# Kernel tuning notes

Hardware: AMD Instinct MI355X
Metric: run time of the kernel (lower is better)

## Reference

```python
import jax, jax.numpy as jnp
import numpy as np

LOG2 = float(np.log(2.0))

def ssp(x):
    # shifted softplus used throughout SchNet
    return jax.nn.softplus(x) - LOG2

def setup_inputs() -> dict:
    key = jax.random.key(0)
    ks = jax.random.split(key, 12)
    B, Na, Nn, G, F = 16, 512, 64, 25, 128
    s = 0.05
    return {
        "x": jax.random.normal(ks[0], (B, Na, F), jnp.float32),
        "r_ij": jax.random.uniform(ks[1], (B, Na, Nn), jnp.float32),
        "f_ij": jax.random.uniform(ks[2], (B, Na, Nn, G), jnp.float32),
        "neighbours": jax.random.randint(ks[3], (B, Na, Nn), 0, Na),
        "pairwise_mask": jax.random.uniform(ks[4], (B, Na, Nn), jnp.float32),
        "W_in2f": jax.random.normal(ks[5], (F, F), jnp.float32) * s,
        "W_f1": jax.random.normal(ks[6], (G, F), jnp.float32) * s,
        "b_f1": jnp.zeros((F,), jnp.float32),
        "W_f2": jax.random.normal(ks[7], (F, F), jnp.float32) * s,
        "b_f2": jnp.zeros((F,), jnp.float32),
        "W_out": jax.random.normal(ks[8], (F, F), jnp.float32) * s,
        "b_out": jnp.zeros((F,), jnp.float32),
    }

def reference(x, r_ij, f_ij, neighbours, pairwise_mask,
              W_in2f, W_f1, b_f1, W_f2, b_f2, W_out, b_out):
    # filter_network: Dense(G->F, ssp) -> Dense(F->F)
    W = jnp.einsum('bang,gf->banf', f_ij, W_f1) + b_f1  # [B,Na,Nn,F]
    W = ssp(W)
    W = jnp.einsum('banf,fg->bang', W, W_f2) + b_f2
    # in2f (no bias)
    y = jnp.einsum('bai,if->baf', x, W_in2f)  # [B,Na,F]
    B, Na, Nn = neighbours.shape
    # gather neighbor features: y[b, neighbours[b,a,n], :]
    nbh = neighbours.reshape(B, Na * Nn, 1)
    g = jnp.take_along_axis(y, nbh, axis=1).reshape(B, Na, Nn, -1)
    # filter multiply, mask, aggregate over neighbor axis (sum, no mean)
    agg = jnp.sum(g * W * pairwise_mask[..., None], axis=2)  # [B,Na,F]
    # f2out with shifted softplus activation
    out = ssp(jnp.einsum('baf,fo->bao', agg, W_out) + b_out)
    return out
```

## Files before the change

kernel.cpp:

```cpp
#include <hip/hip_runtime.h>

typedef __attribute__((ext_vector_type(8))) short bf16x8;
typedef __attribute__((ext_vector_type(4))) float f32x4;
typedef __attribute__((ext_vector_type(4))) unsigned int u32x4;

#define LOG2F 0.69314718055994531f
#define LOG2EF 1.4426950408889634f

#define NB 16
#define NA 512
#define NN 64
#define NG 25
#define NF 128

__device__ __forceinline__ unsigned short f2bf(float x) {
    __bf16 h = (__bf16)x;
    return __builtin_bit_cast(unsigned short, h);
}
__device__ __forceinline__ float ssp2(float s) {
    float t = __builtin_amdgcn_exp2f(s);
    return fmaf(__builtin_amdgcn_logf(1.0f + t), LOG2F, -LOG2F);
}

__device__ __forceinline__ void stage_fij(const float* fp, float* sfij, int w, int lane) {
    const char* fb = (const char*)fp;
    __builtin_amdgcn_global_load_lds(
        (const __attribute__((address_space(1))) void*)(fb + w * 1024 + lane * 16),
        (__attribute__((address_space(3))) void*)((char*)sfij + w * 1024), 16, 0, 0);
    if (w < 2) {
        __builtin_amdgcn_global_load_lds(
            (const __attribute__((address_space(1))) void*)(fb + (w + 4) * 1024 + lane * 16),
            (__attribute__((address_space(3))) void*)((char*)sfij + (w + 4) * 1024), 16, 0, 0);
    }
    if (w == 3) {
        __builtin_amdgcn_global_load_lds(
            (const __attribute__((address_space(1))) void*)(fb + 6144 + lane * 4),
            (__attribute__((address_space(3))) void*)((char*)sfij + 6144), 4, 0, 0);
    }
}

#define FRAG_WF1 0
#define FRAG_WF2 4096
#define FRAG_WIN 20480
#define FRAG_WOUT 36864
#define B1S_OFF   106496
#define YBF_OFF   107008
#define AGG_OFF   2204160

__global__ __launch_bounds__(256) void k_prep(
    const float* __restrict__ Wf1, const float* __restrict__ Wf2,
    const float* __restrict__ Win, const float* __restrict__ Wout,
    const float* __restrict__ b1, char* __restrict__ ws)
{
    unsigned short* frag = (unsigned short*)ws;
    int idx = blockIdx.x * 256 + threadIdx.x;
    if (idx < 4096) {
        int j = idx & 7, lane = (idx >> 3) & 63, tc = idx >> 9;
        int f1 = tc * 16 + (lane & 15);
        int g  = (lane >> 4) * 8 + j;
        frag[idx] = (g < NG) ? f2bf(Wf1[g * NF + f1] * LOG2EF) : (unsigned short)0;
    } else if (idx < 20480) {
        int t = idx - 4096;
        int j = t & 7, lane = (t >> 3) & 63, ks = (t >> 9) & 3, tn = t >> 11;
        int f = tn * 16 + (lane & 15);
        int k = ks * 32 + (lane >> 4) * 8 + j;
        frag[idx] = f2bf(Wf2[k * NF + f]);
    } else if (idx < 36864) {
        int t = idx - 20480;
        int j = t & 7, lane = (t >> 3) & 63, ks = (t >> 9) & 3, tn = t >> 11;
        int f = tn * 16 + (lane & 15);
        int k = ks * 32 + (lane >> 4) * 8 + j;
        frag[idx] = f2bf(Win[k * NF + f]);
    } else if (idx < 53248) {
        int t = idx - 36864;
        int j = t & 7, lane = (t >> 3) & 63, ks = (t >> 9) & 3, tn = t >> 11;
        int f = tn * 16 + (lane & 15);
        int k = ks * 32 + (lane >> 4) * 8 + j;
        frag[idx] = f2bf(Wout[k * NF + f]);
    } else if (idx < 53376) {
        ((float*)(ws + B1S_OFF))[idx - 53248] = b1[idx - 53248] * LOG2EF;
    }
}

__global__ __launch_bounds__(256) void k_in2f(
    const float* __restrict__ x, const unsigned short* __restrict__ frag,
    unsigned short* __restrict__ ybf)
{
    const unsigned short* winfrag = frag + FRAG_WIN;
    const int lane = threadIdx.x & 63, w = threadIdx.x >> 6;
    const int rowbase = blockIdx.x * 32;
    f32x4 acc[2][2];
    f32x4 z = {0.f, 0.f, 0.f, 0.f};
    acc[0][0] = z; acc[0][1] = z; acc[1][0] = z; acc[1][1] = z;
#pragma unroll
    for (int ks = 0; ks < 4; ++ks) {
        bf16x8 a[2];
#pragma unroll
        for (int tm = 0; tm < 2; ++tm) {
            int row = rowbase + tm * 16 + (lane & 15);
            int k0  = ks * 32 + (lane >> 4) * 8;
            const float* p = x + (size_t)row * NF + k0;
            float4 v0 = *(const float4*)p;
            float4 v1 = *(const float4*)(p + 4);
            bf16x8 t;
            t[0] = (short)f2bf(v0.x); t[1] = (short)f2bf(v0.y);
            t[2] = (short)f2bf(v0.z); t[3] = (short)f2bf(v0.w);
            t[4] = (short)f2bf(v1.x); t[5] = (short)f2bf(v1.y);
            t[6] = (short)f2bf(v1.z); t[7] = (short)f2bf(v1.w);
            a[tm] = t;
        }
#pragma unroll
        for (int tn = 0; tn < 2; ++tn) {
            bf16x8 bfr = *(const bf16x8*)(winfrag + ((((w * 2 + tn) * 4 + ks) * 64) + lane) * 8);
#pragma unroll
            for (int tm = 0; tm < 2; ++tm)
                acc[tm][tn] = __builtin_amdgcn_mfma_f32_16x16x32_bf16(a[tm], bfr, acc[tm][tn], 0, 0, 0);
        }
    }
#pragma unroll
    for (int tm = 0; tm < 2; ++tm)
#pragma unroll
        for (int tn = 0; tn < 2; ++tn)
#pragma unroll
            for (int r = 0; r < 4; ++r) {
                int row = rowbase + tm * 16 + (lane >> 4) * 4 + r;
                int f   = w * 32 + tn * 16 + (lane & 15);
                ybf[(size_t)row * NF + f] = f2bf(acc[tm][tn][r]);
            }
}

__global__ __launch_bounds__(256, 4) void k_cfconv(
    const float* __restrict__ fij, const int* __restrict__ nbh,
    const float* __restrict__ mask, const float* __restrict__ b1s,
    const float* __restrict__ b2, const unsigned short* __restrict__ frag,
    const unsigned short* __restrict__ ybf, float* __restrict__ agg)
{
    __shared__ alignas(16) float sfij[1600];
    __shared__ alignas(16) unsigned short sW1T[8192];
    __shared__ alignas(16) float smask[128];
    __shared__ alignas(16) int   snbh[128];

    const int tid = threadIdx.x, lane = tid & 63, w = tid >> 6;
    const int g = lane >> 4, lc = lane & 15;
    const int a0 = blockIdx.x * 2;
    const int bidx = a0 >> 9;
    const int fbase = w * 32;
    const int fc0 = fbase + lc;

    if (tid < 128) {
        smask[tid] = mask[(size_t)a0 * NN + tid];
        snbh[tid]  = nbh[(size_t)a0 * NN + tid];
    }

    stage_fij(fij + (size_t)a0 * (NN * NG), sfij, w, lane);

    const unsigned short* wf1frag = frag + FRAG_WF1;
    const unsigned short* wf2frag = frag + FRAG_WF2;
    bf16x8 afr[2], vb[4];
    f32x4  rg[8];
#pragma unroll
    for (int i = 0; i < 2; ++i)
        afr[i] = *(const bf16x8*)(wf1frag + (((2 * w + i) * 64) + lane) * 8);
    f32x4 ci[2];
#pragma unroll
    for (int i = 0; i < 2; ++i)
        ci[i] = *(const f32x4*)(b1s + (2 * w + i) * 16 + g * 4);
    const float bias0 = b2[fc0], bias1 = b2[fc0 + 16];
    const unsigned short* yb = ybf + (size_t)bidx * NA * NF;

    __syncthreads();

#pragma unroll
    for (int a = 0; a < 2; ++a) {
        {
            const int g0 = g * 8;
            const unsigned int m0 = (g == 3) ? 0x0000FFFFu : 0xFFFFFFFFu;
            const unsigned int m1 = (g == 3) ? 0u : 0xFFFFFFFFu;
#pragma unroll
            for (int tn = 0; tn < 4; ++tn) {
                int n = tn * 16 + lc;
                const float* p = sfij + n * NG + g0;
                bf16x8 t;
                t[0] = (short)f2bf(p[0]); t[1] = (short)f2bf(p[1]);
                t[2] = (short)f2bf(p[2]); t[3] = (short)f2bf(p[3]);
                t[4] = (short)f2bf(p[4]); t[5] = (short)f2bf(p[5]);
                t[6] = (short)f2bf(p[6]); t[7] = (short)f2bf(p[7]);
                u32x4 tv = __builtin_bit_cast(u32x4, t);
                tv[0] &= m0; tv[1] &= m1; tv[2] &= m1; tv[3] &= m1;
                vb[tn] = __builtin_bit_cast(bf16x8, tv);
            }
        }

        if (a == 0) {
            __syncthreads();
            stage_fij(fij + (size_t)(a0 + 1) * (NN * NG), sfij, w, lane);
        }

#pragma unroll
        for (int i = 0; i < 2; ++i)
#pragma unroll
            for (int tn = 0; tn < 4; ++tn)
                rg[i * 4 + tn] = __builtin_amdgcn_mfma_f32_16x16x32_bf16(afr[i], vb[tn], ci[i], 0, 0, 0);

#pragma unroll
        for (int i = 0; i < 2; ++i) {
            int c0 = (2 * w + i) * 16 + g * 4;
#pragma unroll
            for (int tn = 0; tn < 4; ++tn) {
                int n = tn * 16 + lc;
                ushort4 pk;
#pragma unroll
                for (int r = 0; r < 4; ++r)
                    ((unsigned short*)&pk)[r] = f2bf(ssp2(rg[i * 4 + tn][r]));
                *(ushort4*)((char*)sW1T + n * 256 + ((c0 * 2) ^ ((n & 7) << 4))) = pk;
            }
        }
        __syncthreads();

#pragma unroll
        for (int tm = 0; tm < 4; ++tm) {
            rg[tm * 2 + 0] = f32x4{bias0, bias0, bias0, bias0};
            rg[tm * 2 + 1] = f32x4{bias1, bias1, bias1, bias1};
        }
#pragma unroll
        for (int ks = 0; ks < 4; ++ks) {
#pragma unroll
            for (int tm = 0; tm < 4; ++tm) {
                int n  = tm * 16 + lc;
                int kb = ks * 64 + g * 16;
                vb[tm] = *(const bf16x8*)((char*)sW1T + n * 256 + (kb ^ ((n & 7) << 4)));
            }
#pragma unroll
            for (int tnl = 0; tnl < 2; ++tnl) {
                int tn = w * 2 + tnl;
                bf16x8 bf2 = *(const bf16x8*)(wf2frag + (((tn * 4 + ks) * 64) + lane) * 8);
#pragma unroll
                for (int tm = 0; tm < 4; ++tm)
                    rg[tm * 2 + tnl] = __builtin_amdgcn_mfma_f32_16x16x32_bf16(vb[tm], bf2, rg[tm * 2 + tnl], 0, 0, 0);
            }
        }

        {
            const float* sm = smask + a * 64;
            const int*   sn = snbh + a * 64;
            float aggv0 = 0.f, aggv1 = 0.f;
#pragma unroll
            for (int tm = 0; tm < 4; ++tm) {
                f32x4 m4 = *(const f32x4*)(sm + tm * 16 + g * 4);
                int4  nb4 = *(const int4*)(sn + tm * 16 + g * 4);
#pragma unroll
                for (int r = 0; r < 4; ++r) {
                    int yrow = (r == 0) ? nb4.x : (r == 1) ? nb4.y : (r == 2) ? nb4.z : nb4.w;
                    const unsigned short* yp = yb + (size_t)yrow * NF + fc0;
                    float y0 = __builtin_bit_cast(float, (unsigned int)yp[0] << 16);
                    float y1 = __builtin_bit_cast(float, (unsigned int)yp[16] << 16);
                    aggv0 = fmaf(rg[tm * 2 + 0][r] * m4[r], y0, aggv0);
                    aggv1 = fmaf(rg[tm * 2 + 1][r] * m4[r], y1, aggv1);
                }
            }
            aggv0 += __shfl_xor(aggv0, 16); aggv1 += __shfl_xor(aggv1, 16);
            aggv0 += __shfl_xor(aggv0, 32); aggv1 += __shfl_xor(aggv1, 32);
            if (lane < 16) {
                float* ap = agg + (size_t)(a0 + a) * NF + fbase;
                ap[lane] = aggv0;
                ap[16 + lane] = aggv1;
            }
        }

        if (a == 0) __syncthreads();
    }
}

__global__ __launch_bounds__(256) void k_out(
    const float* __restrict__ agg, const unsigned short* __restrict__ frag,
    const float* __restrict__ bout, float* __restrict__ out)
{
    const unsigned short* wofrag = frag + FRAG_WOUT;
    const int lane = threadIdx.x & 63, w = threadIdx.x >> 6;
    const int rowbase = blockIdx.x * 32;
    const int f0 = w * 32 + (lane & 15);
    const float bo0 = bout[f0], bo1 = bout[f0 + 16];
    f32x4 acc[2][2];
    acc[0][0] = f32x4{bo0, bo0, bo0, bo0};
    acc[1][0] = f32x4{bo0, bo0, bo0, bo0};
    acc[0][1] = f32x4{bo1, bo1, bo1, bo1};
    acc[1][1] = f32x4{bo1, bo1, bo1, bo1};
#pragma unroll
    for (int ks = 0; ks < 4; ++ks) {
        bf16x8 a[2];
#pragma unroll
        for (int tm = 0; tm < 2; ++tm) {
            int row = rowbase + tm * 16 + (lane & 15);
            int k0  = ks * 32 + (lane >> 4) * 8;
            const float* p = agg + (size_t)row * NF + k0;
            float4 v0 = *(const float4*)p;
            float4 v1 = *(const float4*)(p + 4);
            bf16x8 t;
            t[0] = (short)f2bf(v0.x); t[1] = (short)f2bf(v0.y);
            t[2] = (short)f2bf(v0.z); t[3] = (short)f2bf(v0.w);
            t[4] = (short)f2bf(v1.x); t[5] = (short)f2bf(v1.y);
            t[6] = (short)f2bf(v1.z); t[7] = (short)f2bf(v1.w);
            a[tm] = t;
        }
#pragma unroll
        for (int tn = 0; tn < 2; ++tn) {
            bf16x8 bfr = *(const bf16x8*)(wofrag + ((((w * 2 + tn) * 4 + ks) * 64) + lane) * 8);
#pragma unroll
            for (int tm = 0; tm < 2; ++tm)
                acc[tm][tn] = __builtin_amdgcn_mfma_f32_16x16x32_bf16(a[tm], bfr, acc[tm][tn], 0, 0, 0);
        }
    }
    float lg2 = LOG2EF;
#pragma unroll
    for (int tm = 0; tm < 2; ++tm)
#pragma unroll
        for (int tn = 0; tn < 2; ++tn)
#pragma unroll
            for (int r = 0; r < 4; ++r) {
                int row = rowbase + tm * 16 + (lane >> 4) * 4 + r;
                int f   = w * 32 + tn * 16 + (lane & 15);
                out[(size_t)row * NF + f] = ssp2(acc[tm][tn][r] * lg2);
            }
}

extern "C" void kernel_launch(void* const* d_in, const int* in_sizes, int n_in,
                              void* d_out, int out_size, void* d_ws, size_t ws_size,
                              hipStream_t stream)
{
    (void)in_sizes; (void)n_in; (void)out_size; (void)ws_size;
    const float* x    = (const float*)d_in[0];
    const float* fij  = (const float*)d_in[2];
    const int*   nbh  = (const int*)d_in[3];
    const float* mask = (const float*)d_in[4];
    const float* Win  = (const float*)d_in[5];
    const float* Wf1  = (const float*)d_in[6];
    const float* b1   = (const float*)d_in[7];
    const float* Wf2  = (const float*)d_in[8];
    const float* b2   = (const float*)d_in[9];
    const float* Wout = (const float*)d_in[10];
    const float* bout = (const float*)d_in[11];
    float* out = (float*)d_out;

    char* ws = (char*)d_ws;
    unsigned short* frag = (unsigned short*)ws;
    const float*    b1s  = (const float*)(ws + B1S_OFF);
    unsigned short* ybf  = (unsigned short*)(ws + YBF_OFF);
    float*          agg  = (float*)(ws + AGG_OFF);

    k_prep  <<<209,  256, 0, stream>>>(Wf1, Wf2, Win, Wout, b1, ws);
    k_in2f  <<<256,  256, 0, stream>>>(x, frag, ybf);
    k_cfconv<<<4096, 256, 0, stream>>>(fij, nbh, mask, b1s, b2, frag, ybf, agg);
    k_out   <<<256,  256, 0, stream>>>(agg, frag, bout, out);
}
```

Baseline: 59.49 us.

## Process both atoms concurrently with two waves per atom in cfconv kernel

```diff
diff --git a/kernel.cpp b/kernel.cpp
--- a/kernel.cpp
+++ b/kernel.cpp
@@ -13,29 +13,35 @@
 #define NG 25
 #define NF 128
 
+#define AS1 __attribute__((address_space(1)))
+#define AS3 __attribute__((address_space(3)))
+
 __device__ __forceinline__ unsigned short f2bf(float x) {
     __bf16 h = (__bf16)x;
     return __builtin_bit_cast(unsigned short, h);
 }
+__device__ __forceinline__ float bf2f(unsigned short h) {
+    union { unsigned int u; float f; } c; c.u = ((unsigned int)h) << 16;
+    return c.f;
+}
 __device__ __forceinline__ float ssp2(float s) {
     float t = __builtin_amdgcn_exp2f(s);
     return fmaf(__builtin_amdgcn_logf(1.0f + t), LOG2F, -LOG2F);
 }
 
-__device__ __forceinline__ void stage_fij(const float* fp, float* sfij, int w, int lane) {
+__device__ __forceinline__ void stage_fij2(const float* fp, char* dst, int wp, int lane) {
     const char* fb = (const char*)fp;
-    __builtin_amdgcn_global_load_lds(
-        (const __attribute__((address_space(1))) void*)(fb + w * 1024 + lane * 16),
-        (__attribute__((address_space(3))) void*)((char*)sfij + w * 1024), 16, 0, 0);
-    if (w < 2) {
+#pragma unroll
+    for (int c = 0; c < 3; ++c) {
+        int chunk = wp * 3 + c;
         __builtin_amdgcn_global_load_lds(
-            (const __attribute__((address_space(1))) void*)(fb + (w + 4) * 1024 + lane * 16),
-            (__attribute__((address_space(3))) void*)((char*)sfij + (w + 4) * 1024), 16, 0, 0);
-    }
-    if (w == 3) {
+            (const AS1 void*)(fb + chunk * 1024 + lane * 16),
+            (AS3 void*)(dst + chunk * 1024), 16, 0, 0);
+    }
+    if (wp == 1) {
         __builtin_amdgcn_global_load_lds(
-            (const __attribute__((address_space(1))) void*)(fb + 6144 + lane * 4),
-            (__attribute__((address_space(3))) void*)((char*)sfij + 6144), 4, 0, 0);
+            (const AS1 void*)(fb + 6144 + lane * 4),
+            (AS3 void*)(dst + 6144), 4, 0, 0);
     }
 }
 
@@ -135,139 +141,147 @@
     const float* __restrict__ b2, const unsigned short* __restrict__ frag,
     const unsigned short* __restrict__ ybf, float* __restrict__ agg)
 {
-    __shared__ alignas(16) float sfij[1600];
-    __shared__ alignas(16) unsigned short sW1T[8192];
-    __shared__ alignas(16) float smask[128];
-    __shared__ alignas(16) int   snbh[128];
+    __shared__ alignas(16) char smem[33792];
+    float* smask = (float*)(smem + 32768);
+    int*   snbh  = (int*)(smem + 33280);
 
     const int tid = threadIdx.x, lane = tid & 63, w = tid >> 6;
+    const int wp = w & 1, at = w >> 1;
     const int g = lane >> 4, lc = lane & 15;
     const int a0 = blockIdx.x * 2;
+    const int atom = a0 + at;
     const int bidx = a0 >> 9;
-    const int fbase = w * 32;
-    const int fc0 = fbase + lc;
 
     if (tid < 128) {
         smask[tid] = mask[(size_t)a0 * NN + tid];
         snbh[tid]  = nbh[(size_t)a0 * NN + tid];
     }
 
-    stage_fij(fij + (size_t)a0 * (NN * NG), sfij, w, lane);
+    char* myW1T = smem + at * 16384;
+    stage_fij2(fij + (size_t)atom * (NN * NG), myW1T, wp, lane);
 
     const unsigned short* wf1frag = frag + FRAG_WF1;
     const unsigned short* wf2frag = frag + FRAG_WF2;
-    bf16x8 afr[2], vb[4];
-    f32x4  rg[8];
-#pragma unroll
-    for (int i = 0; i < 2; ++i)
-        afr[i] = *(const bf16x8*)(wf1frag + (((2 * w + i) * 64) + lane) * 8);
-    f32x4 ci[2];
-#pragma unroll
-    for (int i = 0; i < 2; ++i)
-        ci[i] = *(const f32x4*)(b1s + (2 * w + i) * 16 + g * 4);
-    const float bias0 = b2[fc0], bias1 = b2[fc0 + 16];
-    const unsigned short* yb = ybf + (size_t)bidx * NA * NF;
+    bf16x8 afr[4];
+#pragma unroll
+    for (int i = 0; i < 4; ++i)
+        afr[i] = *(const bf16x8*)(wf1frag + (((wp * 4 + i) * 64) + lane) * 8);
+    float bb[4];
+#pragma unroll
+    for (int tf = 0; tf < 4; ++tf)
+        bb[tf] = b2[wp * 64 + tf * 16 + lc];
 
     __syncthreads();
 
-#pragma unroll
-    for (int a = 0; a < 2; ++a) {
-        {
-            const int g0 = g * 8;
-            const unsigned int m0 = (g == 3) ? 0x0000FFFFu : 0xFFFFFFFFu;
-            const unsigned int m1 = (g == 3) ? 0u : 0xFFFFFFFFu;
-#pragma unroll
-            for (int tn = 0; tn < 4; ++tn) {
-                int n = tn * 16 + lc;
-                const float* p = sfij + n * NG + g0;
-                bf16x8 t;
-                t[0] = (short)f2bf(p[0]); t[1] = (short)f2bf(p[1]);
-                t[2] = (short)f2bf(p[2]); t[3] = (short)f2bf(p[3]);
-                t[4] = (short)f2bf(p[4]); t[5] = (short)f2bf(p[5]);
-                t[6] = (short)f2bf(p[6]); t[7] = (short)f2bf(p[7]);
-                u32x4 tv = __builtin_bit_cast(u32x4, t);
-                tv[0] &= m0; tv[1] &= m1; tv[2] &= m1; tv[3] &= m1;
-                vb[tn] = __builtin_bit_cast(bf16x8, tv);
-            }
-        }
-
-        if (a == 0) {
-            __syncthreads();
-            stage_fij(fij + (size_t)(a0 + 1) * (NN * NG), sfij, w, lane);
-        }
-
-#pragma unroll
-        for (int i = 0; i < 2; ++i)
+    bf16x8 vb[4];
+    {
+        const float* sfij = (const float*)myW1T;
+        const int g0 = g * 8;
+        const unsigned int m0 = (g == 3) ? 0x0000FFFFu : 0xFFFFFFFFu;
+        const unsigned int m1 = (g == 3) ? 0u : 0xFFFFFFFFu;
+#pragma unroll
+        for (int tn = 0; tn < 4; ++tn) {
+            int n = tn * 16 + lc;
+            const float* p = sfij + n * NG + g0;
+            bf16x8 t;
+            t[0] = (short)f2bf(p[0]); t[1] = (short)f2bf(p[1]);
+            t[2] = (short)f2bf(p[2]); t[3] = (short)f2bf(p[3]);
+            t[4] = (short)f2bf(p[4]); t[5] = (short)f2bf(p[5]);
+            t[6] = (short)f2bf(p[6]); t[7] = (short)f2bf(p[7]);
+            u32x4 tv = __builtin_bit_cast(u32x4, t);
+            tv[0] &= m0; tv[1] &= m1; tv[2] &= m1; tv[3] &= m1;
+            vb[tn] = __builtin_bit_cast(bf16x8, tv);
+        }
+    }
+
+    __syncthreads();
+
+#pragma unroll
+    for (int h = 0; h < 2; ++h) {
+        f32x4 dW[2][4];
+#pragma unroll
+        for (int ii = 0; ii < 2; ++ii) {
+            int it = wp * 4 + h * 2 + ii;
+            f32x4 ci = *(const f32x4*)(b1s + it * 16 + g * 4);
 #pragma unroll
             for (int tn = 0; tn < 4; ++tn)
-                rg[i * 4 + tn] = __builtin_amdgcn_mfma_f32_16x16x32_bf16(afr[i], vb[tn], ci[i], 0, 0, 0);
-
-#pragma unroll
-        for (int i = 0; i < 2; ++i) {
-            int c0 = (2 * w + i) * 16 + g * 4;
+                dW[ii][tn] = __builtin_amdgcn_mfma_f32_16x16x32_bf16(afr[h * 2 + ii], vb[tn], ci, 0, 0, 0);
+        }
+#pragma unroll
+        for (int ii = 0; ii < 2; ++ii) {
+            int c0 = (wp * 4 + h * 2 + ii) * 16 + g * 4;
 #pragma unroll
             for (int tn = 0; tn < 4; ++tn) {
                 int n = tn * 16 + lc;
                 ushort4 pk;
 #pragma unroll
                 for (int r = 0; r < 4; ++r)
-                    ((unsigned short*)&pk)[r] = f2bf(ssp2(rg[i * 4 + tn][r]));
-                *(ushort4*)((char*)sW1T + n * 256 + ((c0 * 2) ^ ((n & 7) << 4))) = pk;
-            }
-        }
-        __syncthreads();
-
-#pragma unroll
-        for (int tm = 0; tm < 4; ++tm) {
-            rg[tm * 2 + 0] = f32x4{bias0, bias0, bias0, bias0};
-            rg[tm * 2 + 1] = f32x4{bias1, bias1, bias1, bias1};
+                    ((unsigned short*)&pk)[r] = f2bf(ssp2(dW[ii][tn][r]));
+                *(ushort4*)(myW1T + n * 256 + ((c0 * 2) ^ ((n & 7) << 4))) = pk;
+            }
+        }
+    }
+    __syncthreads();
+
+    const unsigned short* yb = ybf + (size_t)bidx * NA * NF;
+    const float* sm = smask + at * 64;
+    const int*   sn = snbh + at * 64;
+    float aggv[4] = {0.f, 0.f, 0.f, 0.f};
+#pragma unroll
+    for (int tfh = 0; tfh < 2; ++tfh) {
+        f32x4 acc[2][4];
+#pragma unroll
+        for (int tt = 0; tt < 2; ++tt) {
+            float b = bb[tfh * 2 + tt];
+#pragma unroll
+            for (int tm = 0; tm < 4; ++tm)
+                acc[tt][tm] = f32x4{b, b, b, b};
         }
 #pragma unroll
         for (int ks = 0; ks < 4; ++ks) {
+            bf16x8 va[4];
 #pragma unroll
             for (int tm = 0; tm < 4; ++tm) {
                 int n  = tm * 16 + lc;
                 int kb = ks * 64 + g * 16;
-                vb[tm] = *(const bf16x8*)((char*)sW1T + n * 256 + (kb ^ ((n & 7) << 4)));
-            }
-#pragma unroll
-            for (int tnl = 0; tnl < 2; ++tnl) {
-                int tn = w * 2 + tnl;
-                bf16x8 bf2 = *(const bf16x8*)(wf2frag + (((tn * 4 + ks) * 64) + lane) * 8);
+                va[tm] = *(const bf16x8*)(myW1T + n * 256 + (kb ^ ((n & 7) << 4)));
+            }
+#pragma unroll
+            for (int tt = 0; tt < 2; ++tt) {
+                int tng = wp * 4 + tfh * 2 + tt;
+                bf16x8 bf2 = *(const bf16x8*)(wf2frag + (((tng * 4 + ks) * 64) + lane) * 8);
 #pragma unroll
                 for (int tm = 0; tm < 4; ++tm)
-                    rg[tm * 2 + tnl] = __builtin_amdgcn_mfma_f32_16x16x32_bf16(vb[tm], bf2, rg[tm * 2 + tnl], 0, 0, 0);
-            }
-        }
-
-        {
-            const float* sm = smask + a * 64;
-            const int*   sn = snbh + a * 64;
-            float aggv0 = 0.f, aggv1 = 0.f;
-#pragma unroll
-            for (int tm = 0; tm < 4; ++tm) {
-                f32x4 m4 = *(const f32x4*)(sm + tm * 16 + g * 4);
-                int4  nb4 = *(const int4*)(sn + tm * 16 + g * 4);
-#pragma unroll
-                for (int r = 0; r < 4; ++r) {
-                    int yrow = (r == 0) ? nb4.x : (r == 1) ? nb4.y : (r == 2) ? nb4.z : nb4.w;
-                    const unsigned short* yp = yb + (size_t)yrow * NF + fc0;
-                    float y0 = __builtin_bit_cast(float, (unsigned int)yp[0] << 16);
-                    float y1 = __builtin_bit_cast(float, (unsigned int)yp[16] << 16);
-                    aggv0 = fmaf(rg[tm * 2 + 0][r] * m4[r], y0, aggv0);
-                    aggv1 = fmaf(rg[tm * 2 + 1][r] * m4[r], y1, aggv1);
+                    acc[tt][tm] = __builtin_amdgcn_mfma_f32_16x16x32_bf16(va[tm], bf2, acc[tt][tm], 0, 0, 0);
+            }
+        }
+#pragma unroll
+        for (int tm = 0; tm < 4; ++tm) {
+            f32x4 m4 = *(const f32x4*)(sm + tm * 16 + g * 4);
+            int4  nb4 = *(const int4*)(sn + tm * 16 + g * 4);
+#pragma unroll
+            for (int r = 0; r < 4; ++r) {
+                int yrow = (r == 0) ? nb4.x : (r == 1) ? nb4.y : (r == 2) ? nb4.z : nb4.w;
+                const unsigned short* yp = yb + (size_t)yrow * NF + wp * 64 + lc;
+#pragma unroll
+                for (int tt = 0; tt < 2; ++tt) {
+                    float y = bf2f(yp[(tfh * 2 + tt) * 16]);
+                    aggv[tfh * 2 + tt] = fmaf(acc[tt][tm][r] * m4[r], y, aggv[tfh * 2 + tt]);
                 }
             }
-            aggv0 += __shfl_xor(aggv0, 16); aggv1 += __shfl_xor(aggv1, 16);
-            aggv0 += __shfl_xor(aggv0, 32); aggv1 += __shfl_xor(aggv1, 32);
-            if (lane < 16) {
-                float* ap = agg + (size_t)(a0 + a) * NF + fbase;
-                ap[lane] = aggv0;
-                ap[16 + lane] = aggv1;
-            }
-        }
-
-        if (a == 0) __syncthreads();
+        }
+    }
+
+#pragma unroll
+    for (int tf = 0; tf < 4; ++tf) {
+        aggv[tf] += __shfl_xor(aggv[tf], 16);
+        aggv[tf] += __shfl_xor(aggv[tf], 32);
+    }
+    if (lane < 16) {
+        float* ap = agg + (size_t)atom * NF + wp * 64;
+#pragma unroll
+        for (int tf = 0; tf < 4; ++tf)
+            ap[tf * 16 + lane] = aggv[tf];
     }
 }
 
```

Result: slower. 116.7 us (+96.2%).
